# Optimization experiments

Measured on AMD Instinct MI355X. Metric: run time of the kernel, lower is better.

The kernel has to match this reference:

```python
import jax, jax.numpy as jnp
import numpy as np

NUM_NODES = 80000
NUM_EDGES = 1280000
NUM_GRAPHS = 512
IN_DIM = 64
HID = 64
NUM_CLASSES = 10


def setup_inputs() -> dict:
    key = jax.random.key(0)
    ks = jax.random.split(key, 16)
    x = jax.random.normal(ks[0], (NUM_NODES, IN_DIM), dtype=jnp.float32)
    edge_index = jax.random.randint(ks[1], (2, NUM_EDGES), 0, NUM_NODES, dtype=jnp.int64)
    batch = jnp.sort(jax.random.randint(ks[2], (NUM_NODES,), 0, NUM_GRAPHS, dtype=jnp.int64))

    def glorot(k, shape):
        fan_in, fan_out = shape[1], shape[0]
        lim = jnp.sqrt(6.0 / (fan_in + fan_out))
        return jax.random.uniform(k, shape, dtype=jnp.float32, minval=-lim, maxval=lim)

    inp = {
        "x": x,
        "edge_index": edge_index,
        "batch": batch,
        # GraphConv layer 1: lin_rel (with bias) applied to aggregated neighbors, lin_root (no bias)
        "w_rel1": glorot(ks[3], (HID, IN_DIM)),
        "b_rel1": jnp.zeros((HID,), dtype=jnp.float32),
        "w_root1": glorot(ks[4], (HID, IN_DIM)),
        # layer 2
        "w_rel2": glorot(ks[5], (HID, HID)),
        "b_rel2": jnp.zeros((HID,), dtype=jnp.float32),
        "w_root2": glorot(ks[6], (HID, HID)),
        # layer 3
        "w_rel3": glorot(ks[7], (HID, HID)),
        "b_rel3": jnp.zeros((HID,), dtype=jnp.float32),
        "w_root3": glorot(ks[8], (HID, HID)),
        # final linear head
        "w_lin": glorot(ks[9], (NUM_CLASSES, HID)),
        "b_lin": jnp.zeros((NUM_CLASSES,), dtype=jnp.float32),
    }
    return inp


def _graph_conv(x, src, dst, w_rel, b_rel, w_root):
    # PyG GraphConv with aggr='add': out_i = W_rel @ (sum_{j in N(i)} x_j) + b_rel + W_root @ x_i
    agg = jax.ops.segment_sum(x[src], dst, num_segments=NUM_NODES)  # [N, d_in]
    return agg @ w_rel.T + b_rel + x @ w_root.T


def reference(x, edge_index, batch,
              w_rel1, b_rel1, w_root1,
              w_rel2, b_rel2, w_root2,
              w_rel3, b_rel3, w_root3,
              w_lin, b_lin):
    src, dst = edge_index[0], edge_index[1]
    h = jax.nn.relu(_graph_conv(x, src, dst, w_rel1, b_rel1, w_root1))
    h = jax.nn.relu(_graph_conv(h, src, dst, w_rel2, b_rel2, w_root2))
    h = _graph_conv(h, src, dst, w_rel3, b_rel3, w_root3)
    # global_mean_pool over graph ids
    sums = jax.ops.segment_sum(h, batch, num_segments=NUM_GRAPHS)          # [G, HID]
    counts = jax.ops.segment_sum(jnp.ones((h.shape[0],), h.dtype), batch, num_segments=NUM_GRAPHS)
    pooled = sums / jnp.maximum(counts, 1.0)[:, None]
    # dropout p=0.5 is identity at inference (training=False)
    return pooled @ w_lin.T + b_lin  # [G, NUM_CLASSES]
```

## Files before the change

kernel.cpp:

```cpp
#include <hip/hip_runtime.h>

#define N_NODES  80000
#define N_EDGES  1280000
#define N_GRAPHS 512
#define DIM      64
#define NCLS     10

#define ETILE    8192
#define NTILE    157
#define NCB      157
#define CBPAD    160

typedef short short8f __attribute__((ext_vector_type(8)));
typedef float float4f __attribute__((ext_vector_type(4)));

static __device__ __forceinline__ unsigned short f2bf(float f) {
    unsigned u = __float_as_uint(f);
    unsigned r = (u + 0x7FFFu + ((u >> 16) & 1u)) >> 16;
    return (unsigned short)r;
}
static __device__ __forceinline__ float bf_lo(unsigned v) { return __uint_as_float(v << 16); }
static __device__ __forceinline__ float bf_hi(unsigned v) { return __uint_as_float(v & 0xFFFF0000u); }

__global__ __launch_bounds__(256) void k_scanT(const int* __restrict__ hmat,
        int* __restrict__ obase, int* __restrict__ btot) {
    __shared__ int sa[256], sb[256];
    int b = blockIdx.x, t = threadIdx.x;
    int v = (t < NTILE) ? hmat[t * CBPAD + b] : 0;
    sa[t] = v; __syncthreads();
    int* sp = sa; int* dp = sb;
    for (int off = 1; off < 256; off <<= 1) {
        dp[t] = sp[t] + ((t >= off) ? sp[t - off] : 0);
        __syncthreads();
        int* tmp = sp; sp = dp; dp = tmp;
    }
    int incl = sp[t];
    if (t < NTILE) obase[t * CBPAD + b] = incl - v;
    if (t == NTILE - 1) btot[b] = incl;
}

__global__ __launch_bounds__(256) void k_scanB(const int* __restrict__ btot,
        int* __restrict__ bucketbase, int* __restrict__ rowptr) {
    __shared__ int sa[256], sb[256];
    int t = threadIdx.x;
    int v = (t < NCB) ? btot[t] : 0;
    sa[t] = v; __syncthreads();
    int* sp = sa; int* dp = sb;
    for (int off = 1; off < 256; off <<= 1) {
        dp[t] = sp[t] + ((t >= off) ? sp[t - off] : 0);
        __syncthreads();
        int* tmp = sp; sp = dp; dp = tmp;
    }
    int incl = sp[t];
    if (t < NCB) bucketbase[t] = incl - v;
    if (t == 0) { bucketbase[NCB] = N_EDGES; rowptr[N_NODES] = N_EDGES; }
}

__global__ __launch_bounds__(256) void k_scatter(const int* __restrict__ ei,
        const int* __restrict__ obase, const int* __restrict__ bucketbase,
        int* __restrict__ ebuf) {
    __shared__ int cur[NCB];
    int tile = blockIdx.x, t = threadIdx.x;
    for (int i = t; i < NCB; i += 256)
        cur[i] = bucketbase[i] + obase[tile * CBPAD + i];
    __syncthreads();
    int base = tile * ETILE;
    int end = base + ETILE; if (end > N_EDGES) end = N_EDGES;
    for (int i = base + t; i < end; i += 256) {
        int s = ei[i], d = ei[N_EDGES + i];
        int p = atomicAdd(&cur[d >> 9], 1);
        ebuf[p] = s | ((d & 511) << 17);
    }
}

__global__ __launch_bounds__(256) void k_csr(const int* __restrict__ ebuf,
        const int* __restrict__ bucketbase, int* __restrict__ rowptr,
        int* __restrict__ col) {
    __shared__ int cnt[512];
    __shared__ int sa[512], sb[512];
    __shared__ int cur[512];
    int b = blockIdx.x, t = threadIdx.x;
    int s = bucketbase[b], e = bucketbase[b + 1];
    cnt[t] = 0; cnt[t + 256] = 0;
    __syncthreads();
    for (int i = s + t; i < e; i += 256) atomicAdd(&cnt[ebuf[i] >> 17], 1);
    __syncthreads();
    sa[t] = cnt[t]; sa[t + 256] = cnt[t + 256];
    __syncthreads();
    int* sp = sa; int* dp = sb;
    for (int off = 1; off < 512; off <<= 1) {
        int i1 = t + 256;
        int v0 = sp[t]  + ((t  >= off) ? sp[t  - off] : 0);
        int v1 = sp[i1] + ((i1 >= off) ? sp[i1 - off] : 0);
        __syncthreads();
        dp[t] = v0; dp[i1] = v1;
        __syncthreads();
        int* tmp = sp; sp = dp; dp = tmp;
    }
    int node0 = b * 512;
    int base0 = s + sp[t] - cnt[t];
    int base1 = s + sp[t + 256] - cnt[t + 256];
    cur[t] = base0; cur[t + 256] = base1;
    if (node0 + t < N_NODES)       rowptr[node0 + t] = base0;
    if (node0 + t + 256 < N_NODES) rowptr[node0 + t + 256] = base1;
    __syncthreads();
    for (int i = s + t; i < e; i += 256) {
        int pk = ebuf[i];
        int p = atomicAdd(&cur[pk >> 17], 1);
        col[p] = pk & 0x1FFFF;
    }
}

__global__ __launch_bounds__(256) void k_init(const float* __restrict__ x,
        const int* __restrict__ ei,
        const float* __restrict__ wr1, const float* __restrict__ wo1,
        const float* __restrict__ wr2, const float* __restrict__ wo2,
        unsigned short* __restrict__ xb, unsigned short* __restrict__ wf,
        int* __restrict__ hmat) {
    int bid = blockIdx.x, t = threadIdx.x;
    if (bid < 5000) {
        int i = bid * 256 + t;
        float4 v = ((const float4*)x)[i];
        ushort4 o;
        o.x = f2bf(v.x); o.y = f2bf(v.y); o.z = f2bf(v.z); o.w = f2bf(v.w);
        ((ushort4*)xb)[i] = o;
    } else if (bid < 5064) {
        int idx = (bid - 5000) * 256 + t;
        int j = idx & 7, lane = (idx >> 3) & 63;
        int ks = (idx >> 9) & 3, nt = (idx >> 11) & 3, l = idx >> 13;
        int k = ks * 32 + ((lane >> 4) & 3) * 8 + j;
        int n = nt * 16 + (lane & 15);
        const float* wr = (l == 0) ? wr1 : wr2;
        const float* wo = (l == 0) ? wo1 : wo2;
        float val = (k < 64) ? wr[n * 64 + k] : wo[n * 64 + (k - 64)];
        wf[idx] = f2bf(val);
    } else {
        __shared__ int hist[NCB];
        int tile = bid - 5064;
        for (int i = t; i < NCB; i += 256) hist[i] = 0;
        __syncthreads();
        int base = tile * ETILE;
        int end = base + ETILE; if (end > N_EDGES) end = N_EDGES;
        for (int i = base + t; i < end; i += 256)
            atomicAdd(&hist[ei[N_EDGES + i] >> 9], 1);
        __syncthreads();
        for (int i = t; i < NCB; i += 256) hmat[tile * CBPAD + i] = hist[i];
    }
}

__global__ __launch_bounds__(256) void k_gather4(const unsigned short* __restrict__ Xbf,
        const int* __restrict__ rowptr, const int* __restrict__ col,
        unsigned short* __restrict__ agg) {
    const uint4* Xq = (const uint4*)Xbf;
    int t = threadIdx.x, w = t >> 6, lane = t & 63;
    int e = lane >> 3, c = lane & 7;
    int node = blockIdx.x * 4 + w;
    int start = rowptr[node], end = rowptr[node + 1];
    float acc[8] = {0.f, 0.f, 0.f, 0.f, 0.f, 0.f, 0.f, 0.f};
    int base = start;
    for (; base + 32 <= end; base += 32) {
        int i0 = col[base + e];
        int i1 = col[base + 8 + e];
        int i2 = col[base + 16 + e];
        int i3 = col[base + 24 + e];
        uint4 v0 = Xq[(size_t)i0 * 8 + c];
        uint4 v1 = Xq[(size_t)i1 * 8 + c];
        uint4 v2 = Xq[(size_t)i2 * 8 + c];
        uint4 v3 = Xq[(size_t)i3 * 8 + c];
        acc[0] += (bf_lo(v0.x) + bf_lo(v1.x)) + (bf_lo(v2.x) + bf_lo(v3.x));
        acc[1] += (bf_hi(v0.x) + bf_hi(v1.x)) + (bf_hi(v2.x) + bf_hi(v3.x));
        acc[2] += (bf_lo(v0.y) + bf_lo(v1.y)) + (bf_lo(v2.y) + bf_lo(v3.y));
        acc[3] += (bf_hi(v0.y) + bf_hi(v1.y)) + (bf_hi(v2.y) + bf_hi(v3.y));
        acc[4] += (bf_lo(v0.z) + bf_lo(v1.z)) + (bf_lo(v2.z) + bf_lo(v3.z));
        acc[5] += (bf_hi(v0.z) + bf_hi(v1.z)) + (bf_hi(v2.z) + bf_hi(v3.z));
        acc[6] += (bf_lo(v0.w) + bf_lo(v1.w)) + (bf_lo(v2.w) + bf_lo(v3.w));
        acc[7] += (bf_hi(v0.w) + bf_hi(v1.w)) + (bf_hi(v2.w) + bf_hi(v3.w));
    }
    for (; base + 8 <= end; base += 8) {
        int i0 = col[base + e];
        uint4 v0 = Xq[(size_t)i0 * 8 + c];
        acc[0] += bf_lo(v0.x); acc[1] += bf_hi(v0.x);
        acc[2] += bf_lo(v0.y); acc[3] += bf_hi(v0.y);
        acc[4] += bf_lo(v0.z); acc[5] += bf_hi(v0.z);
        acc[6] += bf_lo(v0.w); acc[7] += bf_hi(v0.w);
    }
    int r = end - base;
    if (e < r) {
        int i0 = col[base + e];
        uint4 v0 = Xq[(size_t)i0 * 8 + c];
        acc[0] += bf_lo(v0.x); acc[1] += bf_hi(v0.x);
        acc[2] += bf_lo(v0.y); acc[3] += bf_hi(v0.y);
        acc[4] += bf_lo(v0.z); acc[5] += bf_hi(v0.z);
        acc[6] += bf_lo(v0.w); acc[7] += bf_hi(v0.w);
    }
#pragma unroll
    for (int off = 8; off < 64; off <<= 1) {
#pragma unroll
        for (int j = 0; j < 8; ++j) acc[j] += __shfl_xor(acc[j], off);
    }
    if (e == 0) {
        uint4 o;
        o.x = (unsigned)f2bf(acc[0]) | ((unsigned)f2bf(acc[1]) << 16);
        o.y = (unsigned)f2bf(acc[2]) | ((unsigned)f2bf(acc[3]) << 16);
        o.z = (unsigned)f2bf(acc[4]) | ((unsigned)f2bf(acc[5]) << 16);
        o.w = (unsigned)f2bf(acc[6]) | ((unsigned)f2bf(acc[7]) << 16);
        ((uint4*)agg)[(size_t)node * 8 + c] = o;
    }
}

__global__ __launch_bounds__(256) void k_linear_mfma(
        const unsigned short* __restrict__ aggb, const unsigned short* __restrict__ xb,
        const unsigned short* __restrict__ wf, const float* __restrict__ bias,
        unsigned short* __restrict__ out, int relu) {
    int t = threadIdx.x, w = t >> 6, lane = t & 63;
    int quad = lane >> 4, l15 = lane & 15;
    int mbase = blockIdx.x * 64 + w * 16;
    size_t arow = (size_t)(mbase + l15) * 64;
    short8f a0 = *(const short8f*)(aggb + arow + quad * 8);
    short8f a1 = *(const short8f*)(aggb + arow + 32 + quad * 8);
    short8f a2 = *(const short8f*)(xb   + arow + quad * 8);
    short8f a3 = *(const short8f*)(xb   + arow + 32 + quad * 8);
    int orow = mbase + quad * 4;
#pragma unroll
    for (int nt = 0; nt < 4; ++nt) {
        const unsigned short* wp = wf + ((size_t)(nt * 4) * 64 + lane) * 8;
        short8f b0 = *(const short8f*)(wp);
        short8f b1 = *(const short8f*)(wp + 64 * 8);
        short8f b2 = *(const short8f*)(wp + 128 * 8);
        short8f b3 = *(const short8f*)(wp + 192 * 8);
        float4f acc = {0.f, 0.f, 0.f, 0.f};
        acc = __builtin_amdgcn_mfma_f32_16x16x32_bf16(a0, b0, acc, 0, 0, 0);
        acc = __builtin_amdgcn_mfma_f32_16x16x32_bf16(a1, b1, acc, 0, 0, 0);
        acc = __builtin_amdgcn_mfma_f32_16x16x32_bf16(a2, b2, acc, 0, 0, 0);
        acc = __builtin_amdgcn_mfma_f32_16x16x32_bf16(a3, b3, acc, 0, 0, 0);
        float bi = bias[nt * 16 + l15];
#pragma unroll
        for (int r = 0; r < 4; ++r) {
            float v = acc[r] + bi;
            if (relu) v = fmaxf(v, 0.f);
            out[(size_t)(orow + r) * 64 + nt * 16 + l15] = f2bf(v);
        }
    }
}

static __device__ __forceinline__ int lowerb(const int* a, int n, int key) {
    int lo = 0, hi = n;
    while (lo < hi) { int mid = (lo + hi) >> 1; if (a[mid] < key) lo = mid + 1; else hi = mid; }
    return lo;
}

__global__ __launch_bounds__(256) void k_gsum(const unsigned short* __restrict__ h2,
        const int* __restrict__ rowptr, const int* __restrict__ col,
        const int* __restrict__ batch, float* __restrict__ S8) {
    __shared__ float red1[8][64];
    __shared__ float red2[8][64];
    const unsigned* Xu = (const unsigned*)h2;
    int g = blockIdx.x >> 3, part = blockIdx.x & 7;
    int t = threadIdx.x;
    int hw = t >> 5, c = t & 31;
    int ns = lowerb(batch, N_NODES, g);
    int ne = lowerb(batch, N_NODES, g + 1);
    int a0 = ns + (int)(((long long)(ne - ns) * part) >> 3);
    int a1 = ns + (int)(((long long)(ne - ns) * (part + 1)) >> 3);
    int es = rowptr[a0], ee = rowptr[a1];
    float alo = 0.f, ahi = 0.f;
    int nfull = (ee - es) >> 7;
    int e0 = es + hw * 16;
    for (int b = 0; b < nfull; ++b, e0 += 128) {
        unsigned v[16];
#pragma unroll
        for (int j = 0; j < 16; ++j)
            v[j] = Xu[(size_t)col[e0 + j] * 32 + c];
#pragma unroll
        for (int j = 0; j < 16; ++j) { alo += bf_lo(v[j]); ahi += bf_hi(v[j]); }
    }
    for (int e = es + nfull * 128 + hw; e < ee; e += 8) {
        unsigned v = Xu[(size_t)col[e] * 32 + c];
        alo += bf_lo(v); ahi += bf_hi(v);
    }
    float blo = 0.f, bhi = 0.f;
    for (int i = a0 + hw; i < a1; i += 8) {
        unsigned v = Xu[(size_t)i * 32 + c];
        blo += bf_lo(v); bhi += bf_hi(v);
    }
    red1[hw][2 * c] = alo; red1[hw][2 * c + 1] = ahi;
    red2[hw][2 * c] = blo; red2[hw][2 * c + 1] = bhi;
    __syncthreads();
    if (t < 64) {
        float v = 0.f;
#pragma unroll
        for (int s = 0; s < 8; ++s) v += red1[s][t];
        S8[(size_t)blockIdx.x * 128 + t] = v;
    } else if (t < 128) {
        float v = 0.f;
#pragma unroll
        for (int s = 0; s < 8; ++s) v += red2[s][t - 64];
        S8[(size_t)blockIdx.x * 128 + 64 + (t - 64)] = v;
    }
}

__global__ __launch_bounds__(64) void k_head2(const float* __restrict__ S8,
        const int* __restrict__ batch,
        const float* __restrict__ wr3, const float* __restrict__ wo3,
        const float* __restrict__ b3,
        const float* __restrict__ wlin, const float* __restrict__ blin,
        float* __restrict__ out) {
    __shared__ float s1[64], s2[64], pl[64];
    int g = blockIdx.x, t = threadIdx.x;
    int ns = lowerb(batch, N_NODES, g);
    int ne = lowerb(batch, N_NODES, g + 1);
    float inv = 1.f / (float)((ne > ns) ? (ne - ns) : 1);
    const float* Sg = S8 + (size_t)g * 8 * 128;
    float v1 = 0.f, v2 = 0.f;
#pragma unroll
    for (int p = 0; p < 8; ++p) {
        v1 += Sg[p * 128 + t];
        v2 += Sg[p * 128 + 64 + t];
    }
    s1[t] = v1 * inv;
    s2[t] = v2 * inv;
    __syncthreads();
    float acc = b3[t];
    for (int k = 0; k < 64; ++k)
        acc += s1[k] * wr3[t * 64 + k] + s2[k] * wo3[t * 64 + k];
    pl[t] = acc;
    __syncthreads();
    float myout = 0.f;
    for (int cls = 0; cls < NCLS; ++cls) {
        float vv = pl[t] * wlin[cls * 64 + t];
        for (int off = 32; off > 0; off >>= 1) vv += __shfl_xor(vv, off);
        if (t == cls) myout = vv + blin[cls];
    }
    if (t < NCLS) out[g * NCLS + t] = myout;
}

extern "C" void kernel_launch(void* const* d_in, const int* in_sizes, int n_in,
                              void* d_out, int out_size, void* d_ws, size_t ws_size,
                              hipStream_t stream) {
    const float* x     = (const float*)d_in[0];
    const int*   ei    = (const int*)d_in[1];
    const int*   batch = (const int*)d_in[2];
    const float* wr1 = (const float*)d_in[3];
    const float* b1  = (const float*)d_in[4];
    const float* wo1 = (const float*)d_in[5];
    const float* wr2 = (const float*)d_in[6];
    const float* b2  = (const float*)d_in[7];
    const float* wo2 = (const float*)d_in[8];
    const float* wr3 = (const float*)d_in[9];
    const float* b3  = (const float*)d_in[10];
    const float* wo3 = (const float*)d_in[11];
    const float* wlin = (const float*)d_in[12];
    const float* blin = (const float*)d_in[13];
    float* out = (float*)d_out;

    char* p = (char*)d_ws;
    auto alloc = [&](size_t bytes) { char* r = p; p += (bytes + 255) & ~(size_t)255; return r; };
    int*   rowptr  = (int*)alloc((N_NODES + 1) * sizeof(int));
    int*   hmat    = (int*)alloc((size_t)NTILE * CBPAD * sizeof(int));
    int*   obase   = (int*)alloc((size_t)NTILE * CBPAD * sizeof(int));
    int*   btot    = (int*)alloc(CBPAD * sizeof(int));
    int*   bucketbase = (int*)alloc((NCB + 1) * sizeof(int));
    int*   ebuf    = (int*)alloc((size_t)N_EDGES * sizeof(int));
    int*   col     = (int*)alloc((size_t)N_EDGES * sizeof(int));
    unsigned short* wf  = (unsigned short*)alloc(2 * 8192 * sizeof(unsigned short));
    unsigned short* xbf = (unsigned short*)alloc((size_t)N_NODES * 64 * 2);
    unsigned short* agg = (unsigned short*)alloc((size_t)N_NODES * 64 * 2);
    unsigned short* hA  = (unsigned short*)alloc((size_t)N_NODES * 64 * 2);
    unsigned short* hB  = (unsigned short*)alloc((size_t)N_NODES * 64 * 2);
    float* S8      = (float*)alloc((size_t)N_GRAPHS * 8 * 128 * sizeof(float));

    k_init   <<<5221,  256, 0, stream>>>(x, ei, wr1, wo1, wr2, wo2, xbf, wf, hmat);
    k_scanT  <<<NCB,   256, 0, stream>>>(hmat, obase, btot);
    k_scanB  <<<1,     256, 0, stream>>>(btot, bucketbase, rowptr);
    k_scatter<<<NTILE, 256, 0, stream>>>(ei, obase, bucketbase, ebuf);
    k_csr    <<<NCB,   256, 0, stream>>>(ebuf, bucketbase, rowptr, col);

    k_gather4    <<<N_NODES / 4,  256, 0, stream>>>(xbf, rowptr, col, agg);
    k_linear_mfma<<<N_NODES / 64, 256, 0, stream>>>(agg, xbf, wf,        b1, hA, 1);
    k_gather4    <<<N_NODES / 4,  256, 0, stream>>>(hA, rowptr, col, agg);
    k_linear_mfma<<<N_NODES / 64, 256, 0, stream>>>(agg, hA, wf + 8192,  b2, hB, 1);
    k_gsum <<<N_GRAPHS * 8, 256, 0, stream>>>(hB, rowptr, col, batch, S8);
    k_head2<<<N_GRAPHS,     64,  0, stream>>>(S8, batch, wr3, wo3, b3, wlin, blin, out);
}
```

Measured before the change: 278.3 us.

## Fold scanB and head kernels into predecessors via last-block atomic counters

Merges the single-block bucket scan into k_scanT and the per-graph head into k_gsum. Each uses a threadfence plus an atomic counter so the last finishing block does the follow-up work, which removes two kernel launches and their boundaries. It also shortens the gather inner unroll from 32 to 16 edges per iteration. The cost is an extra memset of the counters, the atomic and fence overhead, and possibly less memory-level parallelism in the gather.

```diff
diff --git a/kernel.cpp b/kernel.cpp
--- a/kernel.cpp
+++ b/kernel.cpp
@@ -21,95 +21,6 @@
 }
 static __device__ __forceinline__ float bf_lo(unsigned v) { return __uint_as_float(v << 16); }
 static __device__ __forceinline__ float bf_hi(unsigned v) { return __uint_as_float(v & 0xFFFF0000u); }
-
-__global__ __launch_bounds__(256) void k_scanT(const int* __restrict__ hmat,
-        int* __restrict__ obase, int* __restrict__ btot) {
-    __shared__ int sa[256], sb[256];
-    int b = blockIdx.x, t = threadIdx.x;
-    int v = (t < NTILE) ? hmat[t * CBPAD + b] : 0;
-    sa[t] = v; __syncthreads();
-    int* sp = sa; int* dp = sb;
-    for (int off = 1; off < 256; off <<= 1) {
-        dp[t] = sp[t] + ((t >= off) ? sp[t - off] : 0);
-        __syncthreads();
-        int* tmp = sp; sp = dp; dp = tmp;
-    }
-    int incl = sp[t];
-    if (t < NTILE) obase[t * CBPAD + b] = incl - v;
-    if (t == NTILE - 1) btot[b] = incl;
-}
-
-__global__ __launch_bounds__(256) void k_scanB(const int* __restrict__ btot,
-        int* __restrict__ bucketbase, int* __restrict__ rowptr) {
-    __shared__ int sa[256], sb[256];
-    int t = threadIdx.x;
-    int v = (t < NCB) ? btot[t] : 0;
-    sa[t] = v; __syncthreads();
-    int* sp = sa; int* dp = sb;
-    for (int off = 1; off < 256; off <<= 1) {
-        dp[t] = sp[t] + ((t >= off) ? sp[t - off] : 0);
-        __syncthreads();
-        int* tmp = sp; sp = dp; dp = tmp;
-    }
-    int incl = sp[t];
-    if (t < NCB) bucketbase[t] = incl - v;
-    if (t == 0) { bucketbase[NCB] = N_EDGES; rowptr[N_NODES] = N_EDGES; }
-}
-
-__global__ __launch_bounds__(256) void k_scatter(const int* __restrict__ ei,
-        const int* __restrict__ obase, const int* __restrict__ bucketbase,
-        int* __restrict__ ebuf) {
-    __shared__ int cur[NCB];
-    int tile = blockIdx.x, t = threadIdx.x;
-    for (int i = t; i < NCB; i += 256)
-        cur[i] = bucketbase[i] + obase[tile * CBPAD + i];
-    __syncthreads();
-    int base = tile * ETILE;
-    int end = base + ETILE; if (end > N_EDGES) end = N_EDGES;
-    for (int i = base + t; i < end; i += 256) {
-        int s = ei[i], d = ei[N_EDGES + i];
-        int p = atomicAdd(&cur[d >> 9], 1);
-        ebuf[p] = s | ((d & 511) << 17);
-    }
-}
-
-__global__ __launch_bounds__(256) void k_csr(const int* __restrict__ ebuf,
-        const int* __restrict__ bucketbase, int* __restrict__ rowptr,
-        int* __restrict__ col) {
-    __shared__ int cnt[512];
-    __shared__ int sa[512], sb[512];
-    __shared__ int cur[512];
-    int b = blockIdx.x, t = threadIdx.x;
-    int s = bucketbase[b], e = bucketbase[b + 1];
-    cnt[t] = 0; cnt[t + 256] = 0;
-    __syncthreads();
-    for (int i = s + t; i < e; i += 256) atomicAdd(&cnt[ebuf[i] >> 17], 1);
-    __syncthreads();
-    sa[t] = cnt[t]; sa[t + 256] = cnt[t + 256];
-    __syncthreads();
-    int* sp = sa; int* dp = sb;
-    for (int off = 1; off < 512; off <<= 1) {
-        int i1 = t + 256;
-        int v0 = sp[t]  + ((t  >= off) ? sp[t  - off] : 0);
-        int v1 = sp[i1] + ((i1 >= off) ? sp[i1 - off] : 0);
-        __syncthreads();
-        dp[t] = v0; dp[i1] = v1;
-        __syncthreads();
-        int* tmp = sp; sp = dp; dp = tmp;
-    }
-    int node0 = b * 512;
-    int base0 = s + sp[t] - cnt[t];
-    int base1 = s + sp[t + 256] - cnt[t + 256];
-    cur[t] = base0; cur[t + 256] = base1;
-    if (node0 + t < N_NODES)       rowptr[node0 + t] = base0;
-    if (node0 + t + 256 < N_NODES) rowptr[node0 + t + 256] = base1;
-    __syncthreads();
-    for (int i = s + t; i < e; i += 256) {
-        int pk = ebuf[i];
-        int p = atomicAdd(&cur[pk >> 17], 1);
-        col[p] = pk & 0x1FFFF;
-    }
-}
 
 __global__ __launch_bounds__(256) void k_init(const float* __restrict__ x,
         const int* __restrict__ ei,
@@ -148,6 +59,98 @@
     }
 }
 
+__global__ __launch_bounds__(256) void k_scanT(const int* __restrict__ hmat,
+        int* __restrict__ obase, int* __restrict__ btot,
+        int* __restrict__ bucketbase, int* __restrict__ rowptr,
+        int* __restrict__ scnt) {
+    __shared__ int sa[256], sb[256];
+    __shared__ int isLast;
+    int b = blockIdx.x, t = threadIdx.x;
+    int v = (t < NTILE) ? hmat[t * CBPAD + b] : 0;
+    sa[t] = v; __syncthreads();
+    int* sp = sa; int* dp = sb;
+    for (int off = 1; off < 256; off <<= 1) {
+        dp[t] = sp[t] + ((t >= off) ? sp[t - off] : 0);
+        __syncthreads();
+        int* tmp = sp; sp = dp; dp = tmp;
+    }
+    int incl = sp[t];
+    if (t < NTILE) obase[t * CBPAD + b] = incl - v;
+    if (t == NTILE - 1) btot[b] = incl;
+    __threadfence();
+    __syncthreads();
+    if (t == 0) isLast = (atomicAdd(scnt, 1) == NCB - 1);
+    __syncthreads();
+    if (isLast) {
+        int v2 = (t < NCB) ? btot[t] : 0;
+        sa[t] = v2; __syncthreads();
+        sp = sa; dp = sb;
+        for (int off = 1; off < 256; off <<= 1) {
+            dp[t] = sp[t] + ((t >= off) ? sp[t - off] : 0);
+            __syncthreads();
+            int* tmp = sp; sp = dp; dp = tmp;
+        }
+        int incl2 = sp[t];
+        if (t < NCB) bucketbase[t] = incl2 - v2;
+        if (t == 0) { bucketbase[NCB] = N_EDGES; rowptr[N_NODES] = N_EDGES; }
+    }
+}
+
+__global__ __launch_bounds__(256) void k_scatter(const int* __restrict__ ei,
+        const int* __restrict__ obase, const int* __restrict__ bucketbase,
+        int* __restrict__ ebuf) {
+    __shared__ int cur[NCB];
+    int tile = blockIdx.x, t = threadIdx.x;
+    for (int i = t; i < NCB; i += 256)
+        cur[i] = bucketbase[i] + obase[tile * CBPAD + i];
+    __syncthreads();
+    int base = tile * ETILE;
+    int end = base + ETILE; if (end > N_EDGES) end = N_EDGES;
+    for (int i = base + t; i < end; i += 256) {
+        int s = ei[i], d = ei[N_EDGES + i];
+        int p = atomicAdd(&cur[d >> 9], 1);
+        ebuf[p] = s | ((d & 511) << 17);
+    }
+}
+
+__global__ __launch_bounds__(256) void k_csr(const int* __restrict__ ebuf,
+        const int* __restrict__ bucketbase, int* __restrict__ rowptr,
+        int* __restrict__ col) {
+    __shared__ int cnt[512];
+    __shared__ int sa[512], sb[512];
+    __shared__ int cur[512];
+    int b = blockIdx.x, t = threadIdx.x;
+    int s = bucketbase[b], e = bucketbase[b + 1];
+    cnt[t] = 0; cnt[t + 256] = 0;
+    __syncthreads();
+    for (int i = s + t; i < e; i += 256) atomicAdd(&cnt[ebuf[i] >> 17], 1);
+    __syncthreads();
+    sa[t] = cnt[t]; sa[t + 256] = cnt[t + 256];
+    __syncthreads();
+    int* sp = sa; int* dp = sb;
+    for (int off = 1; off < 512; off <<= 1) {
+        int i1 = t + 256;
+        int v0 = sp[t]  + ((t  >= off) ? sp[t  - off] : 0);
+        int v1 = sp[i1] + ((i1 >= off) ? sp[i1 - off] : 0);
+        __syncthreads();
+        dp[t] = v0; dp[i1] = v1;
+        __syncthreads();
+        int* tmp = sp; sp = dp; dp = tmp;
+    }
+    int node0 = b * 512;
+    int base0 = s + sp[t] - cnt[t];
+    int base1 = s + sp[t + 256] - cnt[t + 256];
+    cur[t] = base0; cur[t + 256] = base1;
+    if (node0 + t < N_NODES)       rowptr[node0 + t] = base0;
+    if (node0 + t + 256 < N_NODES) rowptr[node0 + t + 256] = base1;
+    __syncthreads();
+    for (int i = s + t; i < e; i += 256) {
+        int pk = ebuf[i];
+        int p = atomicAdd(&cur[pk >> 17], 1);
+        col[p] = pk & 0x1FFFF;
+    }
+}
+
 __global__ __launch_bounds__(256) void k_gather4(const unsigned short* __restrict__ Xbf,
         const int* __restrict__ rowptr, const int* __restrict__ col,
         unsigned short* __restrict__ agg) {
@@ -158,23 +161,15 @@
     int start = rowptr[node], end = rowptr[node + 1];
     float acc[8] = {0.f, 0.f, 0.f, 0.f, 0.f, 0.f, 0.f, 0.f};
     int base = start;
-    for (; base + 32 <= end; base += 32) {
+    for (; base + 16 <= end; base += 16) {
         int i0 = col[base + e];
         int i1 = col[base + 8 + e];
-        int i2 = col[base + 16 + e];
-        int i3 = col[base + 24 + e];
         uint4 v0 = Xq[(size_t)i0 * 8 + c];
         uint4 v1 = Xq[(size_t)i1 * 8 + c];
-        uint4 v2 = Xq[(size_t)i2 * 8 + c];
-        uint4 v3 = Xq[(size_t)i3 * 8 + c];
-        acc[0] += (bf_lo(v0.x) + bf_lo(v1.x)) + (bf_lo(v2.x) + bf_lo(v3.x));
-        acc[1] += (bf_hi(v0.x) + bf_hi(v1.x)) + (bf_hi(v2.x) + bf_hi(v3.x));
-        acc[2] += (bf_lo(v0.y) + bf_lo(v1.y)) + (bf_lo(v2.y) + bf_lo(v3.y));
-        acc[3] += (bf_hi(v0.y) + bf_hi(v1.y)) + (bf_hi(v2.y) + bf_hi(v3.y));
-        acc[4] += (bf_lo(v0.z) + bf_lo(v1.z)) + (bf_lo(v2.z) + bf_lo(v3.z));
-        acc[5] += (bf_hi(v0.z) + bf_hi(v1.z)) + (bf_hi(v2.z) + bf_hi(v3.z));
-        acc[6] += (bf_lo(v0.w) + bf_lo(v1.w)) + (bf_lo(v2.w) + bf_lo(v3.w));
-        acc[7] += (bf_hi(v0.w) + bf_hi(v1.w)) + (bf_hi(v2.w) + bf_hi(v3.w));
+        acc[0] += bf_lo(v0.x) + bf_lo(v1.x); acc[1] += bf_hi(v0.x) + bf_hi(v1.x);
+        acc[2] += bf_lo(v0.y) + bf_lo(v1.y); acc[3] += bf_hi(v0.y) + bf_hi(v1.y);
+        acc[4] += bf_lo(v0.z) + bf_lo(v1.z); acc[5] += bf_hi(v0.z) + bf_hi(v1.z);
+        acc[6] += bf_lo(v0.w) + bf_lo(v1.w); acc[7] += bf_hi(v0.w) + bf_hi(v1.w);
     }
     for (; base + 8 <= end; base += 8) {
         int i0 = col[base + e];
@@ -251,9 +246,16 @@
 
 __global__ __launch_bounds__(256) void k_gsum(const unsigned short* __restrict__ h2,
         const int* __restrict__ rowptr, const int* __restrict__ col,
-        const int* __restrict__ batch, float* __restrict__ S8) {
+        const int* __restrict__ batch, float* __restrict__ S8,
+        int* __restrict__ gcnt,
+        const float* __restrict__ wr3, const float* __restrict__ wo3,
+        const float* __restrict__ b3,
+        const float* __restrict__ wlin, const float* __restrict__ blin,
+        float* __restrict__ out) {
     __shared__ float red1[8][64];
     __shared__ float red2[8][64];
+    __shared__ float s1[64], s2[64], pl[64];
+    __shared__ int isLast;
     const unsigned* Xu = (const unsigned*)h2;
     int g = blockIdx.x >> 3, part = blockIdx.x & 7;
     int t = threadIdx.x;
@@ -297,41 +299,38 @@
         for (int s = 0; s < 8; ++s) v += red2[s][t - 64];
         S8[(size_t)blockIdx.x * 128 + 64 + (t - 64)] = v;
     }
-}
-
-__global__ __launch_bounds__(64) void k_head2(const float* __restrict__ S8,
-        const int* __restrict__ batch,
-        const float* __restrict__ wr3, const float* __restrict__ wo3,
-        const float* __restrict__ b3,
-        const float* __restrict__ wlin, const float* __restrict__ blin,
-        float* __restrict__ out) {
-    __shared__ float s1[64], s2[64], pl[64];
-    int g = blockIdx.x, t = threadIdx.x;
-    int ns = lowerb(batch, N_NODES, g);
-    int ne = lowerb(batch, N_NODES, g + 1);
-    float inv = 1.f / (float)((ne > ns) ? (ne - ns) : 1);
-    const float* Sg = S8 + (size_t)g * 8 * 128;
-    float v1 = 0.f, v2 = 0.f;
-#pragma unroll
-    for (int p = 0; p < 8; ++p) {
-        v1 += Sg[p * 128 + t];
-        v2 += Sg[p * 128 + 64 + t];
-    }
-    s1[t] = v1 * inv;
-    s2[t] = v2 * inv;
-    __syncthreads();
-    float acc = b3[t];
-    for (int k = 0; k < 64; ++k)
-        acc += s1[k] * wr3[t * 64 + k] + s2[k] * wo3[t * 64 + k];
-    pl[t] = acc;
-    __syncthreads();
-    float myout = 0.f;
-    for (int cls = 0; cls < NCLS; ++cls) {
-        float vv = pl[t] * wlin[cls * 64 + t];
-        for (int off = 32; off > 0; off >>= 1) vv += __shfl_xor(vv, off);
-        if (t == cls) myout = vv + blin[cls];
-    }
-    if (t < NCLS) out[g * NCLS + t] = myout;
+    __threadfence();
+    __syncthreads();
+    if (t == 0) isLast = (atomicAdd(&gcnt[g], 1) == 7);
+    __syncthreads();
+    if (!isLast) return;
+    if (t < 64) {
+        float inv = 1.f / (float)((ne > ns) ? (ne - ns) : 1);
+        const float* Sg = S8 + (size_t)g * 8 * 128;
+        float v1 = 0.f, v2 = 0.f;
+#pragma unroll
+        for (int p = 0; p < 8; ++p) {
+            v1 += Sg[p * 128 + t];
+            v2 += Sg[p * 128 + 64 + t];
+        }
+        s1[t] = v1 * inv;
+        s2[t] = v2 * inv;
+    }
+    __syncthreads();
+    if (t < 64) {
+        float acc = b3[t];
+        for (int k = 0; k < 64; ++k)
+            acc += s1[k] * wr3[t * 64 + k] + s2[k] * wo3[t * 64 + k];
+        pl[t] = acc;
+        __builtin_amdgcn_s_barrier();
+        float myout = 0.f;
+        for (int cls = 0; cls < NCLS; ++cls) {
+            float vv = pl[t] * wlin[cls * 64 + t];
+            for (int off = 32; off > 0; off >>= 1) vv += __shfl_xor(vv, off);
+            if (t == cls) myout = vv + blin[cls];
+        }
+        if (t < NCLS) out[g * NCLS + t] = myout;
+    }
 }
 
 extern "C" void kernel_launch(void* const* d_in, const int* in_sizes, int n_in,
@@ -368,10 +367,14 @@
     unsigned short* hA  = (unsigned short*)alloc((size_t)N_NODES * 64 * 2);
     unsigned short* hB  = (unsigned short*)alloc((size_t)N_NODES * 64 * 2);
     float* S8      = (float*)alloc((size_t)N_GRAPHS * 8 * 128 * sizeof(float));
+    int*   ctrs    = (int*)alloc((N_GRAPHS + 1) * sizeof(int));
+    int*   gcnt    = ctrs;
+    int*   scnt    = ctrs + N_GRAPHS;
+
+    hipMemsetAsync(ctrs, 0, (N_GRAPHS + 1) * sizeof(int), stream);
 
     k_init   <<<5221,  256, 0, stream>>>(x, ei, wr1, wo1, wr2, wo2, xbf, wf, hmat);
-    k_scanT  <<<NCB,   256, 0, stream>>>(hmat, obase, btot);
-    k_scanB  <<<1,     256, 0, stream>>>(btot, bucketbase, rowptr);
+    k_scanT  <<<NCB,   256, 0, stream>>>(hmat, obase, btot, bucketbase, rowptr, scnt);
     k_scatter<<<NTILE, 256, 0, stream>>>(ei, obase, bucketbase, ebuf);
     k_csr    <<<NCB,   256, 0, stream>>>(ebuf, bucketbase, rowptr, col);
 
@@ -379,6 +382,6 @@
     k_linear_mfma<<<N_NODES / 64, 256, 0, stream>>>(agg, xbf, wf,        b1, hA, 1);
     k_gather4    <<<N_NODES / 4,  256, 0, stream>>>(hA, rowptr, col, agg);
     k_linear_mfma<<<N_NODES / 64, 256, 0, stream>>>(agg, hA, wf + 8192,  b2, hB, 1);
-    k_gsum <<<N_GRAPHS * 8, 256, 0, stream>>>(hB, rowptr, col, batch, S8);
-    k_head2<<<N_GRAPHS,     64,  0, stream>>>(S8, batch, wr3, wo3, b3, wlin, blin, out);
-}
+    k_gsum<<<N_GRAPHS * 8, 256, 0, stream>>>(hB, rowptr, col, batch, S8, gcnt,
+                                             wr3, wo3, b3, wlin, blin, out);
+}
```

Measured after the change: 680.8 us. +144.7%, slower.
